# Kernel optimization log

Measured on AMD Instinct MI355X. Metric: run time of the kernel, lower is better.

## Reference

```python
import jax, jax.numpy as jnp
import numpy as np

N = 32768; G = 64; PER = N // G; E = 262144; H = 128; HEADS = 4; DH = H // HEADS

def _leaky(x):
    return jnp.where(x > 0, x, 0.01 * x)

def _bn(x, w, b, eps=1e-5):
    mu = jnp.mean(x, 0)
    var = jnp.var(x, 0)  # biased, as torch BatchNorm1d uses for normalization
    return (x - mu) * jax.lax.rsqrt(var + eps) * w + b

def setup_inputs():
    key = jax.random.key(0)
    ks = jax.random.split(key, 20)
    s = 0.05
    g = jax.random.randint(ks[0], (E,), 0, G)
    src = g * PER + jax.random.randint(ks[1], (E,), 0, PER)
    dst = g * PER + jax.random.randint(ks[2], (E,), 0, PER)
    return {
        'node_fts': jax.random.normal(ks[3], (N, H)),
        'edge_attr': jax.random.normal(ks[4], (E, H)),
        'graph_fts': jax.random.normal(ks[5], (G, H)),
        'hidden': jax.random.normal(ks[6], (N, H)),
        'W_ee': jax.random.normal(ks[7], (H, H)) * s, 'b_ee': jnp.zeros((H,)),
        'M0': jax.random.normal(ks[8], (6 * H, H)) * s,
        'M1': jax.random.normal(ks[9], (H, H)) * s,
        'M2': jax.random.normal(ks[10], (H, H)) * s,
        'M3': jax.random.normal(ks[11], (H, H)) * s,
        'U1': jax.random.normal(ks[12], (2 * H, H)) * s,
        'U2': jax.random.normal(ks[13], (H, H)) * s,
        'Wqkv': jax.random.normal(ks[14], (H, 3 * H)) * s, 'bqkv': jnp.zeros((3 * H,)),
        'Wo': jax.random.normal(ks[15], (H, H)) * s, 'bo': jnp.zeros((H,)),
        'bn1_w': jnp.ones((H,)), 'bn1_b': jnp.zeros((H,)),
        'bn2_w': jnp.ones((H,)), 'bn2_b': jnp.zeros((H,)),
        'bn3_w': jnp.ones((H,)), 'bn3_b': jnp.zeros((H,)),
        'W1': jax.random.normal(ks[16], (H, 2 * H)) * s, 'b1': jnp.zeros((2 * H,)),
        'W2': jax.random.normal(ks[17], (2 * H, H)) * s, 'b2': jnp.zeros((H,)),
        'edge_index': jnp.stack([src, dst]),
        'batch': jnp.arange(N, dtype=jnp.int32) // PER,
    }

def _forward(node_fts, edge_attr, graph_fts, hidden, W_ee, b_ee, M0, M1, M2, M3,
             U1, U2, Wqkv, bqkv, Wo, bo, bn1_w, bn1_b, bn2_w, bn2_b,
             bn3_w, bn3_b, W1, b1, W2, b2, edge_index, batch):
    src, dst = edge_index[0], edge_index[1]
    ea = edge_attr @ W_ee + b_ee                            # GPS.edge_emb  [E,H]
    z = jnp.concatenate([node_fts, hidden], axis=-1)        # [N,2H]
    gfi = graph_fts[batch[dst]]                             # graph_fts_i   [E,H]
    # MPNN message: cat(x_i, x_j, edge_attr, graph_fts_i) -> 4-layer MLP, no bias
    m = jnp.concatenate([z[dst], z[src], ea, gfi], axis=-1) # [E,6H]
    m = m @ M0
    m = _leaky(m) @ M1
    m = _leaky(m) @ M2
    m = _leaky(m) @ M3                                      # [E,H]
    agg = jax.ops.segment_max(m, dst, num_segments=N)
    agg = jnp.where(jnp.isfinite(agg), agg, 0.0)            # PyG max-aggr: 0 for empty segments
    h_local = z @ U1 + agg @ U2                             # MPNN.update (use_gate=False)
    h1 = _bn(h_local + node_fts, bn1_w, bn1_b)              # GPSConv residual + norm1
    # global multihead attention over dense per-graph batches (all graphs exactly PER nodes)
    xd = node_fts.reshape(G, PER, H)
    q, k, v = jnp.split(xd @ Wqkv + bqkv, 3, axis=-1)
    q = q.reshape(G, PER, HEADS, DH).transpose(0, 2, 1, 3)
    k = k.reshape(G, PER, HEADS, DH).transpose(0, 2, 1, 3)
    v = v.reshape(G, PER, HEADS, DH).transpose(0, 2, 1, 3)
    att = jax.nn.softmax(jnp.einsum('ghqd,ghkd->ghqk', q, k) / float(np.sqrt(DH)), axis=-1)
    o = jnp.einsum('ghqk,ghkd->ghqd', att, v).transpose(0, 2, 1, 3).reshape(N, H)
    o = o @ Wo + bo
    h2 = _bn(o + node_fts, bn2_w, bn2_b)                    # residual + norm2
    out = h1 + h2
    out = out + (jax.nn.relu(out @ W1 + b1) @ W2 + b2)      # GPSConv MLP residual
    return _bn(out, bn3_w, bn3_b)                           # norm3

def reference(node_fts, edge_attr, graph_fts, hidden, W_ee, b_ee, M0, M1, M2, M3,
              U1, U2, Wqkv, bqkv, Wo, bo, bn1_w, bn1_b, bn2_w, bn2_b,
              bn3_w, bn3_b, W1, b1, W2, b2, edge_index, batch):
    return _forward(node_fts, edge_attr, graph_fts, hidden, W_ee, b_ee, M0, M1, M2, M3,
                    U1, U2, Wqkv, bqkv, Wo, bo, bn1_w, bn1_b, bn2_w, bn2_b,
                    bn3_w, bn3_b, W1, b1, W2, b2, edge_index, batch)
```

## Files before the change

kernel.cpp:

```cpp
#include <hip/hip_runtime.h>

typedef unsigned short u16;
typedef unsigned int u32;

#define NN 32768
#define EE 262144
#define HH 128
#define INV_N (1.0f / 32768.0f)
#define BN_EPS 1e-5f
#define ENC_NEGINF 0x007FFFFFu

typedef __attribute__((ext_vector_type(8))) __bf16 bf16x8;
typedef __attribute__((ext_vector_type(2))) __bf16 bf16x2;
typedef __attribute__((ext_vector_type(4))) float f32x4;

#define OFF_WEE 0
#define OFF_M0 16384
#define OFF_M1 114688
#define OFF_M2 131072
#define OFF_M3 147456
#define OFF_U 163840
#define OFF_QKV 212992
#define OFF_WO 262144
#define OFF_W1T 278528
#define OFF_W2T 311296
#define WT_ELEMS 344064

#define WS_AGG 0u
#define WS_OUTB 0u
#define WS_Y3 8388608u
#define WS_QKV 16777216u
#define WS_PD 16777216u
#define WS_PS 25165824u
#define WS_Y1 16777216u
#define WS_Y2 25165824u
#define WS_STATS 41943040u
#define WS_WT 41946112u
#define WS_WC 42634240u
#define WS_BV 42667008u
#define WS_G 42667520u

__device__ __forceinline__ float bf2f(u16 u) {
  union { u32 u; float f; } x; x.u = ((u32)u) << 16; return x.f;
}
__device__ __forceinline__ u16 f2bf(float f) {
  union { float f; u32 u; } x; x.f = f;
  return (u16)((x.u + 0x7FFFu + ((x.u >> 16) & 1u)) >> 16);
}
__device__ __forceinline__ u32 pk2bf(float a, float b) {
#if __has_builtin(__builtin_amdgcn_cvt_pk_bf16_f32)
  bf16x2 r = __builtin_amdgcn_cvt_pk_bf16_f32(a, b);
  return __builtin_bit_cast(u32, r);
#else
  return (u32)f2bf(a) | ((u32)f2bf(b) << 16);
#endif
}
__device__ __forceinline__ u32 encf(float f) {
  union { float f; u32 u; } x; x.f = f;
  return (x.u & 0x80000000u) ? ~x.u : (x.u | 0x80000000u);
}
__device__ __forceinline__ float decf(u32 u) {
  union { u32 u; float f; } x;
  x.u = (u & 0x80000000u) ? (u ^ 0x80000000u) : ~u;
  return x.f;
}
__device__ __forceinline__ bf16x8 ld_frag(const u16* p) {
  return __builtin_bit_cast(bf16x8, *(const uint4*)p);
}
__device__ __forceinline__ uint4 pack8(const float* p) {
  float4 x = *(const float4*)p;
  float4 y = *(const float4*)(p + 4);
  return make_uint4(pk2bf(x.x, x.y), pk2bf(x.z, x.w), pk2bf(y.x, y.y),
                    pk2bf(y.z, y.w));
}

template <int NCT>
__device__ __forceinline__ void mfma_step(const u16* As, int astride, int ka,
                                          const u16* Ws, int wstride, int kw,
                                          f32x4* acc, int lane, int wrow) {
  const int q = lane >> 4, cl = lane & 15;
  bf16x8 a = ld_frag(As + (wrow + cl) * astride + ka + q * 8);
#pragma unroll
  for (int ct = 0; ct < NCT; ++ct) {
    bf16x8 b = ld_frag(Ws + (ct * 16 + cl) * wstride + kw + q * 8);
    acc[ct] = __builtin_amdgcn_mfma_f32_16x16x32_bf16(a, b, acc[ct], 0, 0, 0);
  }
}

template <int NCT>
__device__ __forceinline__ void mfma_chunk128(const u16* A0, const u16* A1,
                                              const u16* Ws, int wstride,
                                              f32x4* acc, int lane, int wrow) {
  mfma_step<NCT>(A0, 72, 0, Ws, wstride, 0, acc, lane, wrow);
  mfma_step<NCT>(A0, 72, 32, Ws, wstride, 32, acc, lane, wrow);
  mfma_step<NCT>(A1, 72, 0, Ws, wstride, 64, acc, lane, wrow);
  mfma_step<NCT>(A1, 72, 32, Ws, wstride, 96, acc, lane, wrow);
}

__device__ __forceinline__ void stageA64f(u16* dst, const float* src, int rs, int tid) {
#pragma unroll
  for (int i = 0; i < 2; ++i) {
    int idx = tid + i * 256, r = idx >> 3, s = idx & 7;
    *(uint4*)(dst + r * 72 + s * 8) = pack8(src + (size_t)r * rs + s * 8);
  }
}
__device__ __forceinline__ void stageA64(u16* dst, const u16* src, int rs, int tid) {
#pragma unroll
  for (int i = 0; i < 2; ++i) {
    int idx = tid + i * 256, r = idx >> 3, s = idx & 7;
    *(uint4*)(dst + r * 72 + s * 8) = *(const uint4*)(src + (size_t)r * rs + s * 8);
  }
}
__device__ __forceinline__ void stageA128(u16* dst, const u16* src, int tid) {
#pragma unroll
  for (int i = 0; i < 4; ++i) {
    int idx = tid + i * 256, r = idx >> 4, s = idx & 15;
    *(uint4*)(dst + r * 136 + s * 8) = *(const uint4*)(src + (size_t)r * HH + s * 8);
  }
}
template <int NR, int KW, int DS>
__device__ __forceinline__ void stageW(u16* dst, const u16* wt, int K, int koff, int tid) {
  constexpr int SEGS = KW / 8;
  constexpr int ITER = NR * SEGS / 256;
#pragma unroll
  for (int i = 0; i < ITER; ++i) {
    int idx = tid + i * 256;
    int c = idx / SEGS, s = idx % SEGS;
    *(uint4*)(dst + c * DS + s * 8) = *(const uint4*)(wt + (size_t)c * K + koff + s * 8);
  }
}
__device__ __forceinline__ void stage_agg(u16* dst, const u32* src, int tid) {
#pragma unroll
  for (int i = 0; i < 2; ++i) {
    int idx = tid + i * 256, r = idx >> 3, s = idx & 7;
    const u32* p = src + (size_t)r * HH + s * 8;
    u32 o[4];
#pragma unroll
    for (int j = 0; j < 4; ++j) {
      u32 u0 = p[2 * j], u1 = p[2 * j + 1];
      float f0 = (u0 == ENC_NEGINF) ? 0.f : decf(u0);
      float f1 = (u1 == ENC_NEGINF) ? 0.f : decf(u1);
      o[j] = pk2bf(f0, f1);
    }
    *(uint4*)(dst + r * 72 + s * 8) = make_uint4(o[0], o[1], o[2], o[3]);
  }
}


__global__ __launch_bounds__(256) void k_init(u32* __restrict__ agg,
                                              float* __restrict__ stats) {
  int gid = blockIdx.x * 256 + threadIdx.x;
  *(uint4*)(agg + (size_t)gid * 4) =
      make_uint4(ENC_NEGINF, ENC_NEGINF, ENC_NEGINF, ENC_NEGINF);
  if (gid < 768) stats[gid] = 0.f;
}

__global__ __launch_bounds__(256) void k_transpose(
    const float* w_ee, const float* m0, const float* m1, const float* m2,
    const float* m3, const float* u1, const float* u2, const float* wqkv,
    const float* wo, const float* w1, const float* w2, u16* __restrict__ wt) {
  const float* src; int K, C, ds, dk; size_t doff;
  switch (blockIdx.y) {
    case 0: src = w_ee; K = 128; C = 128; doff = OFF_WEE; ds = 128; dk = 0; break;
    case 1: src = m0; K = 768; C = 128; doff = OFF_M0; ds = 768; dk = 0; break;
    case 2: src = m1; K = 128; C = 128; doff = OFF_M1; ds = 128; dk = 0; break;
    case 3: src = m2; K = 128; C = 128; doff = OFF_M2; ds = 128; dk = 0; break;
    case 4: src = m3; K = 128; C = 128; doff = OFF_M3; ds = 128; dk = 0; break;
    case 5: src = u1; K = 256; C = 128; doff = OFF_U; ds = 384; dk = 0; break;
    case 6: src = u2; K = 128; C = 128; doff = OFF_U; ds = 384; dk = 256; break;
    case 7: src = wqkv; K = 128; C = 384; doff = OFF_QKV; ds = 128; dk = 0; break;
    case 8: src = wo; K = 128; C = 128; doff = OFF_WO; ds = 128; dk = 0; break;
    case 9: src = w1; K = 128; C = 256; doff = OFF_W1T; ds = 128; dk = 0; break;
    default: src = w2; K = 256; C = 128; doff = OFF_W2T; ds = 256; dk = 0; break;
  }
  int gid = blockIdx.x * 256 + threadIdx.x;
  if (gid < K * C) {
    int k = gid / C, c = gid - k * C;
    wt[doff + (size_t)c * ds + dk + k] = f2bf(src[gid]);
  }
}

__global__ __launch_bounds__(256) void k_prep(const float* __restrict__ b_ee,
                                              const float* __restrict__ graph_fts,
                                              const u16* __restrict__ wt,
                                              u16* __restrict__ wc,
                                              float* __restrict__ bv,
                                              float* __restrict__ G) {
  const int b = blockIdx.x, tid = threadIdx.x;
  if (b < 64) {
    int idx = b * 256 + tid, c = idx >> 7, k = idx & 127;
    const u16* m0 = wt + OFF_M0 + (size_t)c * 768 + 512;
    const u16* we = wt + OFF_WEE + k;
    float s = 0.f;
#pragma unroll 4
    for (int j = 0; j < 128; ++j) s += bf2f(we[j * 128]) * bf2f(m0[j]);
    wc[(size_t)c * 128 + k] = f2bf(s);
  } else if (b < 96) {
    int idx = (b - 64) * 256 + tid, g = idx >> 7, c = idx & 127;
    const u16* m0 = wt + OFF_M0 + (size_t)c * 768 + 640;
    const float* gf = graph_fts + (size_t)g * 128;
    float s = 0.f;
#pragma unroll 4
    for (int j = 0; j < 128; ++j) s += gf[j] * bf2f(m0[j]);
    G[(size_t)g * 128 + c] = s;
  } else if (tid < 128) {
    const u16* m0 = wt + OFF_M0 + (size_t)tid * 768 + 512;
    float s = 0.f;
#pragma unroll 4
    for (int j = 0; j < 128; ++j) s += b_ee[j] * bf2f(m0[j]);
    bv[tid] = s;
  }
}

__global__ __launch_bounds__(256) void k_pd(const float* __restrict__ nf,
                                            const float* __restrict__ hid,
                                            const float* __restrict__ bv,
                                            const float* __restrict__ G,
                                            const u16* __restrict__ wt,
                                            u16* __restrict__ pd,
                                            u16* __restrict__ ps) {
  __shared__ u16 sA0[64 * 72], sA1[64 * 72], sW[128 * 136];
  const int tid = threadIdx.x, lane = tid & 63, w = tid >> 6, wrow = w * 16;
  const int q = lane >> 4, cl = lane & 15;
  const int nb = blockIdx.x * 64, g = nb >> 9;
  const f32x4 fz = {0.f, 0.f, 0.f, 0.f};
  f32x4 accd[8], accs[8];
#pragma unroll
  for (int i = 0; i < 8; ++i) { accd[i] = fz; accs[i] = fz; }
  stageA64f(sA0, nf + (size_t)nb * HH, HH, tid);
  stageA64f(sA1, nf + (size_t)nb * HH + 64, HH, tid);
  stageW<128, 128, 136>(sW, wt + OFF_M0, 768, 0, tid);
  __syncthreads();
  mfma_chunk128<8>(sA0, sA1, sW, 136, accd, lane, wrow);
  __syncthreads();
  stageW<128, 128, 136>(sW, wt + OFF_M0, 768, 256, tid);
  __syncthreads();
  mfma_chunk128<8>(sA0, sA1, sW, 136, accs, lane, wrow);
  __syncthreads();
  stageA64f(sA0, hid + (size_t)nb * HH, HH, tid);
  stageA64f(sA1, hid + (size_t)nb * HH + 64, HH, tid);
  stageW<128, 128, 136>(sW, wt + OFF_M0, 768, 128, tid);
  __syncthreads();
  mfma_chunk128<8>(sA0, sA1, sW, 136, accd, lane, wrow);
  __syncthreads();
  stageW<128, 128, 136>(sW, wt + OFF_M0, 768, 384, tid);
  __syncthreads();
  mfma_chunk128<8>(sA0, sA1, sW, 136, accs, lane, wrow);
#pragma unroll
  for (int ct = 0; ct < 8; ++ct) {
#pragma unroll
    for (int r = 0; r < 4; ++r) {
      int row = wrow + q * 4 + r, col = ct * 16 + cl;
      size_t gi = (size_t)(nb + row) * HH + col;
      pd[gi] = f2bf(accd[ct][r] + G[(size_t)g * 128 + col] + bv[col]);
      ps[gi] = f2bf(accs[ct][r]);
    }
  }
}

#define ES 132
__device__ __forceinline__ void gemm4(f32x4* acc, const u16* sA, const u16* sB,
                                      int lane, int wrow) {
  mfma_step<8>(sA, ES, 0, sB, ES, 0, acc, lane, wrow);
  mfma_step<8>(sA, ES, 32, sB, ES, 32, acc, lane, wrow);
  mfma_step<8>(sA, ES, 64, sB, ES, 64, acc, lane, wrow);
  mfma_step<8>(sA, ES, 96, sB, ES, 96, acc, lane, wrow);
}
__device__ __forceinline__ void stageB(u16* sB, const u16* src, int tid) {
#pragma unroll
  for (int i = 0; i < 8; ++i) {
    int idx = tid + i * 256, c = idx >> 4, s = idx & 15;
    *(uint4*)(sB + c * ES + s * 8) = *(const uint4*)(src + (size_t)c * 128 + s * 8);
  }
}

__global__ __launch_bounds__(256, 3) void k_edge(
    const float* __restrict__ edge_attr, const u16* __restrict__ wc,
    const u16* __restrict__ pd, const u16* __restrict__ ps,
    const u16* __restrict__ wt, const int* __restrict__ ei,
    u32* __restrict__ agg) {
  __shared__ u16 sB[128 * ES];
  __shared__ u16 sA[64 * ES];
  __shared__ int sSrc[64], sDst[64];
  const int tid = threadIdx.x, lane = tid & 63, w = tid >> 6, wrow = w * 16;
  const int q = lane >> 4, cl = lane & 15;
  const int e0 = blockIdx.x * 64;
  if (tid < 64) {
    sSrc[tid] = ei[e0 + tid];
    sDst[tid] = ei[EE + e0 + tid];
  }
  {
    int r = tid >> 2, s = tid & 3;
    const float* p = edge_attr + (size_t)(e0 + r) * HH + s * 32;
#pragma unroll
    for (int k = 0; k < 4; ++k)
      *(uint4*)(sA + r * ES + s * 32 + k * 8) = pack8(p + k * 8);
  }
  stageB(sB, wc, tid);
  __syncthreads();
  const f32x4 fz = {0.f, 0.f, 0.f, 0.f};
  f32x4 acc[8];
#pragma unroll
  for (int i = 0; i < 8; ++i) acc[i] = fz;
  gemm4(acc, sA, sB, lane, wrow);
  __syncthreads();
  {
    int r = tid >> 2, s = tid & 3;
    const u16* prow = pd + (size_t)sDst[r] * HH + s * 32;
    const u16* srow = ps + (size_t)sSrc[r] * HH + s * 32;
#pragma unroll
    for (int k = 0; k < 4; ++k) {
      uint4 a = *(const uint4*)(prow + k * 8);
      uint4 b = *(const uint4*)(srow + k * 8);
      u32 ra[4] = {a.x, a.y, a.z, a.w}, rb[4] = {b.x, b.y, b.z, b.w};
      u32 o[4];
#pragma unroll
      for (int j = 0; j < 4; ++j) {
        float lo = bf2f((u16)ra[j]) + bf2f((u16)rb[j]);
        float hi = bf2f((u16)(ra[j] >> 16)) + bf2f((u16)(rb[j] >> 16));
        o[j] = pk2bf(lo, hi);
      }
      *(uint4*)(sA + r * ES + s * 32 + k * 8) = make_uint4(o[0], o[1], o[2], o[3]);
    }
  }
  stageB(sB, wt + OFF_M1, tid);
  __syncthreads();
#pragma unroll
  for (int ct = 0; ct < 8; ++ct)
#pragma unroll
    for (int r = 0; r < 4; ++r) {
      int off = (wrow + q * 4 + r) * ES + ct * 16 + cl;
      float v = acc[ct][r] + bf2f(sA[off]);
      v = v > 0.f ? v : 0.01f * v;
      sA[off] = f2bf(v);
    }
#pragma unroll
  for (int i = 0; i < 8; ++i) acc[i] = fz;
  gemm4(acc, sA, sB, lane, wrow);
  __syncthreads();
  stageB(sB, wt + OFF_M2, tid);
  __syncthreads();
#pragma unroll
  for (int ct = 0; ct < 8; ++ct)
#pragma unroll
    for (int r = 0; r < 4; ++r) {
      float v = acc[ct][r];
      v = v > 0.f ? v : 0.01f * v;
      sA[(wrow + q * 4 + r) * ES + ct * 16 + cl] = f2bf(v);
    }
#pragma unroll
  for (int i = 0; i < 8; ++i) acc[i] = fz;
  gemm4(acc, sA, sB, lane, wrow);
  __syncthreads();
  stageB(sB, wt + OFF_M3, tid);
  __syncthreads();
#pragma unroll
  for (int ct = 0; ct < 8; ++ct)
#pragma unroll
    for (int r = 0; r < 4; ++r) {
      float v = acc[ct][r];
      v = v > 0.f ? v : 0.01f * v;
      sA[(wrow + q * 4 + r) * ES + ct * 16 + cl] = f2bf(v);
    }
#pragma unroll
  for (int i = 0; i < 8; ++i) acc[i] = fz;
  gemm4(acc, sA, sB, lane, wrow);
#pragma unroll
  for (int r = 0; r < 4; ++r) {
    int d_r = sDst[wrow + q * 4 + r];
#pragma unroll
    for (int ct = 0; ct < 8; ++ct)
      atomicMax(&agg[(size_t)d_r * HH + ct * 16 + cl], encf(acc[ct][r]));
  }
}

__global__ __launch_bounds__(256) void k_y1(const float* __restrict__ node_fts,
                                            const float* __restrict__ hidden,
                                            const u32* __restrict__ agg,
                                            const u16* __restrict__ wt,
                                            u16* __restrict__ y1) {
  __shared__ u16 sA0[64 * 72], sA1[64 * 72], sW[128 * 136];
  const int tid = threadIdx.x, lane = tid & 63, w = tid >> 6, wrow = w * 16;
  const int q = lane >> 4, cl = lane & 15;
  const int nb = blockIdx.x * 64;
  const f32x4 fz = {0.f, 0.f, 0.f, 0.f};
  f32x4 acc[8];
#pragma unroll
  for (int i = 0; i < 8; ++i) acc[i] = fz;
  stageA64f(sA0, node_fts + (size_t)nb * HH, HH, tid);
  stageA64f(sA1, node_fts + (size_t)nb * HH + 64, HH, tid);
  stageW<128, 128, 136>(sW, wt + OFF_U, 384, 0, tid);
  __syncthreads();
  mfma_chunk128<8>(sA0, sA1, sW, 136, acc, lane, wrow);
  __syncthreads();
  stageA64f(sA0, hidden + (size_t)nb * HH, HH, tid);
  stageA64f(sA1, hidden + (size_t)nb * HH + 64, HH, tid);
  stageW<128, 128, 136>(sW, wt + OFF_U, 384, 128, tid);
  __syncthreads();
  mfma_chunk128<8>(sA0, sA1, sW, 136, acc, lane, wrow);
  __syncthreads();
  stage_agg(sA0, agg + (size_t)nb * HH, tid);
  stage_agg(sA1, agg + (size_t)nb * HH + 64, tid);
  stageW<128, 128, 136>(sW, wt + OFF_U, 384, 256, tid);
  __syncthreads();
  mfma_chunk128<8>(sA0, sA1, sW, 136, acc, lane, wrow);
#pragma unroll
  for (int ct = 0; ct < 8; ++ct) {
#pragma unroll
    for (int r = 0; r < 4; ++r) {
      int row = wrow + q * 4 + r, col = ct * 16 + cl;
      size_t gi = (size_t)(nb + row) * HH + col;
      y1[gi] = f2bf(acc[ct][r] + node_fts[gi]);
    }
  }
}

__global__ __launch_bounds__(256) void k_qkv(const float* __restrict__ node_fts,
                                             const u16* __restrict__ wt,
                                             const float* __restrict__ bqkv,
                                             u16* __restrict__ qkv) {
  __shared__ u16 sA0[64 * 72], sA1[64 * 72], sW[128 * 136];
  const int tid = threadIdx.x, lane = tid & 63, w = tid >> 6, wrow = w * 16;
  const int q = lane >> 4, cl = lane & 15;
  const int nb = blockIdx.x * 64;
  const f32x4 fz = {0.f, 0.f, 0.f, 0.f};
  stageA64f(sA0, node_fts + (size_t)nb * HH, HH, tid);
  stageA64f(sA1, node_fts + (size_t)nb * HH + 64, HH, tid);
#pragma unroll 1
  for (int cc = 0; cc < 3; ++cc) {
    if (cc) __syncthreads();
    stageW<128, 128, 136>(sW, wt + OFF_QKV + cc * 128 * 128, 128, 0, tid);
    __syncthreads();
    f32x4 acc[8];
#pragma unroll
    for (int i = 0; i < 8; ++i) acc[i] = fz;
    mfma_chunk128<8>(sA0, sA1, sW, 136, acc, lane, wrow);
#pragma unroll
    for (int ct = 0; ct < 8; ++ct) {
#pragma unroll
      for (int r = 0; r < 4; ++r) {
        int row = wrow + q * 4 + r, col = ct * 16 + cl;
        qkv[(size_t)(nb + row) * 384 + cc * 128 + col] =
            f2bf(acc[ct][r] + bqkv[cc * 128 + col]);
      }
    }
  }
}

#define SPW (32 * 136)
__global__ __launch_bounds__(256) void k_attn(const u16* __restrict__ qkv,
                                              u16* __restrict__ oatt) {
  __shared__ u16 sK[128 * 40];
  __shared__ u16 sVt[32 * 136];
  __shared__ u16 sP[4 * SPW];
  const int tid = threadIdx.x, lane = tid & 63, w = tid >> 6;
  const int q = lane >> 4, cl = lane & 15;
  const int bx = blockIdx.x;
  const int g = bx >> 4, h = (bx >> 2) & 3, qt = bx & 3;
  const u16* base = qkv + (size_t)g * 512 * 384;
  const int q0 = qt * 128 + w * 32;
  const float scale = 0.17677669529663687f;
  bf16x8 qa[2];
#pragma unroll
  for (int t = 0; t < 2; ++t)
    qa[t] = ld_frag(base + (size_t)(q0 + t * 16 + cl) * 384 + h * 32 + q * 8);
  const f32x4 fz = {0.f, 0.f, 0.f, 0.f};
  f32x4 accO[2][2];
  float m_[2][4], l_[2][4];
#pragma unroll
  for (int t = 0; t < 2; ++t) {
    accO[t][0] = fz;
    accO[t][1] = fz;
#pragma unroll
    for (int r = 0; r < 4; ++r) {
      m_[t][r] = -3.4e38f;
      l_[t][r] = 0.f;
    }
  }
  u16* myP = sP + w * SPW;
#pragma unroll 1
  for (int kt = 0; kt < 4; ++kt) {
    __syncthreads();
#pragma unroll
    for (int i = 0; i < 2; ++i) {
      int ii = tid + i * 256, r = ii >> 2, s = ii & 3;
      *(uint4*)(sK + r * 40 + s * 8) =
          *(const uint4*)(base + (size_t)(kt * 128 + r) * 384 + 128 + h * 32 + s * 8);
    }
#pragma unroll
    for (int i = 0; i < 2; ++i) {
      int ii = tid + i * 256, r = ii >> 2, s = ii & 3;
      uint4 v = *(const uint4*)(base + (size_t)(kt * 128 + r) * 384 + 256 + h * 32 + s * 8);
      u32 a[4] = {v.x, v.y, v.z, v.w};
#pragma unroll
      for (int j = 0; j < 4; ++j) {
        sVt[(s * 8 + 2 * j) * 136 + r] = (u16)a[j];
        sVt[(s * 8 + 2 * j + 1) * 136 + r] = (u16)(a[j] >> 16);
      }
    }
    __syncthreads();
    f32x4 accS[2][8];
#pragma unroll
    for (int ct = 0; ct < 8; ++ct) {
      bf16x8 b = ld_frag(sK + (ct * 16 + cl) * 40 + q * 8);
      accS[0][ct] = __builtin_amdgcn_mfma_f32_16x16x32_bf16(qa[0], b, fz, 0, 0, 0);
      accS[1][ct] = __builtin_amdgcn_mfma_f32_16x16x32_bf16(qa[1], b, fz, 0, 0, 0);
    }
#pragma unroll
    for (int t = 0; t < 2; ++t) {
#pragma unroll
      for (int r = 0; r < 4; ++r) {
        float mx = accS[t][0][r];
#pragma unroll
        for (int ct = 1; ct < 8; ++ct) mx = fmaxf(mx, accS[t][ct][r]);
        mx = fmaxf(mx, __shfl_xor(mx, 1));
        mx = fmaxf(mx, __shfl_xor(mx, 2));
        mx = fmaxf(mx, __shfl_xor(mx, 4));
        mx = fmaxf(mx, __shfl_xor(mx, 8));
        float mn = fmaxf(m_[t][r], mx * scale);
        float f = __expf(m_[t][r] - mn);
        m_[t][r] = mn;
        float rs = 0.f;
#pragma unroll
        for (int ct = 0; ct < 8; ++ct) {
          float p = __expf(accS[t][ct][r] * scale - mn);
          accS[t][ct][r] = p;
          rs += p;
        }
        rs += __shfl_xor(rs, 1);
        rs += __shfl_xor(rs, 2);
        rs += __shfl_xor(rs, 4);
        rs += __shfl_xor(rs, 8);
        l_[t][r] = l_[t][r] * f + rs;
        accO[t][0][r] *= f;
        accO[t][1][r] *= f;
      }
    }
#pragma unroll
    for (int t = 0; t < 2; ++t)
#pragma unroll
      for (int ct = 0; ct < 8; ++ct)
#pragma unroll
        for (int r = 0; r < 4; ++r)
          myP[(t * 16 + q * 4 + r) * 136 + ct * 16 + cl] = f2bf(accS[t][ct][r]);
#pragma unroll
    for (int kk = 0; kk < 4; ++kk) {
      bf16x8 pa0 = ld_frag(myP + (size_t)cl * 136 + kk * 32 + q * 8);
      bf16x8 pa1 = ld_frag(myP + (size_t)(16 + cl) * 136 + kk * 32 + q * 8);
#pragma unroll
      for (int c = 0; c < 2; ++c) {
        bf16x8 b = ld_frag(sVt + (c * 16 + cl) * 136 + kk * 32 + q * 8);
        accO[0][c] = __builtin_amdgcn_mfma_f32_16x16x32_bf16(pa0, b, accO[0][c], 0, 0, 0);
        accO[1][c] = __builtin_amdgcn_mfma_f32_16x16x32_bf16(pa1, b, accO[1][c], 0, 0, 0);
      }
    }
  }
#pragma unroll
  for (int t = 0; t < 2; ++t)
#pragma unroll
    for (int r = 0; r < 4; ++r) {
      float il = 1.f / l_[t][r];
      int row = g * 512 + q0 + t * 16 + q * 4 + r;
#pragma unroll
      for (int c = 0; c < 2; ++c)
        oatt[(size_t)row * HH + h * 32 + c * 16 + cl] = f2bf(accO[t][c][r] * il);
    }
}

__global__ __launch_bounds__(256) void k_y2(const u16* __restrict__ oatt,
                                            const float* __restrict__ node_fts,
                                            const u16* __restrict__ wt,
                                            const float* __restrict__ bo,
                                            u16* __restrict__ y2) {
  __shared__ u16 sA0[64 * 72], sA1[64 * 72], sW[128 * 136];
  const int tid = threadIdx.x, lane = tid & 63, w = tid >> 6, wrow = w * 16;
  const int q = lane >> 4, cl = lane & 15;
  const int nb = blockIdx.x * 64;
  const f32x4 fz = {0.f, 0.f, 0.f, 0.f};
  f32x4 acc[8];
#pragma unroll
  for (int i = 0; i < 8; ++i) acc[i] = fz;
  stageA64(sA0, oatt + (size_t)nb * HH, HH, tid);
  stageA64(sA1, oatt + (size_t)nb * HH + 64, HH, tid);
  stageW<128, 128, 136>(sW, wt + OFF_WO, 128, 0, tid);
  __syncthreads();
  mfma_chunk128<8>(sA0, sA1, sW, 136, acc, lane, wrow);
#pragma unroll
  for (int ct = 0; ct < 8; ++ct) {
#pragma unroll
    for (int r = 0; r < 4; ++r) {
      int row = wrow + q * 4 + r, col = ct * 16 + cl;
      size_t gi = (size_t)(nb + row) * HH + col;
      y2[gi] = f2bf(acc[ct][r] + bo[col] + node_fts[gi]);
    }
  }
}

__global__ __launch_bounds__(256) void k_stats(const u16* __restrict__ y,
                                               float* __restrict__ sum,
                                               float* __restrict__ sq) {
  const int tid = threadIdx.x, f = tid & 127, rh = tid >> 7;
  const int rb = blockIdx.x * 64;
  float s = 0.f, s2 = 0.f;
  for (int i = 0; i < 32; ++i) {
    float v = bf2f(y[(size_t)(rb + rh + 2 * i) * HH + f]);
    s += v;
    s2 += v * v;
  }
  __shared__ float bs[256], bq[256];
  bs[tid] = s;
  bq[tid] = s2;
  __syncthreads();
  if (tid < 128) {
    atomicAdd(&sum[f], bs[tid] + bs[tid + 128]);
    atomicAdd(&sq[f], bq[tid] + bq[tid + 128]);
  }
}

__global__ __launch_bounds__(256) void k_combine(
    const u16* __restrict__ y1, const u16* __restrict__ y2,
    const float* __restrict__ stats, const float* __restrict__ w1,
    const float* __restrict__ b1, const float* __restrict__ w2,
    const float* __restrict__ b2, u16* __restrict__ outb) {
  int i4 = blockIdx.x * 256 + threadIdx.x;
  uint2 a2 = *(const uint2*)(y1 + (size_t)i4 * 4);
  uint2 b2v = *(const uint2*)(y2 + (size_t)i4 * 4);
  u16 av[4] = {(u16)a2.x, (u16)(a2.x >> 16), (u16)a2.y, (u16)(a2.y >> 16)};
  u16 bv[4] = {(u16)b2v.x, (u16)(b2v.x >> 16), (u16)b2v.y, (u16)(b2v.y >> 16)};
  int f0 = (i4 & 31) * 4;
  u16 o[4];
#pragma unroll
  for (int j = 0; j < 4; ++j) {
    int f = f0 + j;
    float mu1 = stats[f] * INV_N;
    float v1 = stats[128 + f] * INV_N - mu1 * mu1;
    float r1 = rsqrtf(v1 + BN_EPS);
    float mu2 = stats[256 + f] * INV_N;
    float v2 = stats[384 + f] * INV_N - mu2 * mu2;
    float r2 = rsqrtf(v2 + BN_EPS);
    float val = (bf2f(av[j]) - mu1) * r1 * w1[f] + b1[f] +
                (bf2f(bv[j]) - mu2) * r2 * w2[f] + b2[f];
    o[j] = f2bf(val);
  }
  u32 lo2 = (u32)o[0] | ((u32)o[1] << 16);
  u32 hi2 = (u32)o[2] | ((u32)o[3] << 16);
  *(uint2*)(outb + (size_t)i4 * 4) = make_uint2(lo2, hi2);
}

__global__ __launch_bounds__(256) void k_mlp(const u16* __restrict__ outb,
                                             const u16* __restrict__ wt,
                                             const float* __restrict__ b1,
                                             const float* __restrict__ b2,
                                             u16* __restrict__ y3) {
  __shared__ u16 sA[64 * 136];
  __shared__ u16 sW[128 * 136];
  __shared__ u16 sI[64 * 72];
  const int tid = threadIdx.x, lane = tid & 63, w = tid >> 6, wrow = w * 16;
  const int q = lane >> 4, cl = lane & 15;
  const int nb = blockIdx.x * 64;
  const f32x4 fz = {0.f, 0.f, 0.f, 0.f};
  stageA128(sA, outb + (size_t)nb * HH, tid);
  f32x4 acc3[8];
#pragma unroll
  for (int i = 0; i < 8; ++i) acc3[i] = fz;
#pragma unroll 1
  for (int cc = 0; cc < 4; ++cc) {
    __syncthreads();
    stageW<64, 128, 136>(sW, wt + OFF_W1T + cc * 64 * 128, 128, 0, tid);
    __syncthreads();
    f32x4 a1[4];
#pragma unroll
    for (int i = 0; i < 4; ++i) a1[i] = fz;
    mfma_step<4>(sA, 136, 0, sW, 136, 0, a1, lane, wrow);
    mfma_step<4>(sA, 136, 32, sW, 136, 32, a1, lane, wrow);
    mfma_step<4>(sA, 136, 64, sW, 136, 64, a1, lane, wrow);
    mfma_step<4>(sA, 136, 96, sW, 136, 96, a1, lane, wrow);
#pragma unroll
    for (int ct = 0; ct < 4; ++ct) {
      float bias = b1[cc * 64 + ct * 16 + cl];
#pragma unroll
      for (int r = 0; r < 4; ++r) {
        float v = fmaxf(a1[ct][r] + bias, 0.f);
        sI[(wrow + q * 4 + r) * 72 + ct * 16 + cl] = f2bf(v);
      }
    }
    __syncthreads();
    stageW<128, 64, 72>(sW, wt + OFF_W2T, 256, cc * 64, tid);
    __syncthreads();
    mfma_step<8>(sI, 72, 0, sW, 72, 0, acc3, lane, wrow);
    mfma_step<8>(sI, 72, 32, sW, 72, 32, acc3, lane, wrow);
  }
#pragma unroll
  for (int ct = 0; ct < 8; ++ct) {
#pragma unroll
    for (int r = 0; r < 4; ++r) {
      int row = wrow + q * 4 + r, col = ct * 16 + cl;
      size_t gi = (size_t)(nb + row) * HH + col;
      y3[gi] = f2bf(acc3[ct][r] + b2[col] + bf2f(outb[gi]));
    }
  }
}

__global__ __launch_bounds__(256) void k_final(const u16* __restrict__ y3,
                                               const float* __restrict__ sum3,
                                               const float* __restrict__ sq3,
                                               const float* __restrict__ w3,
                                               const float* __restrict__ b3,
                                               float* __restrict__ out) {
  int i4 = blockIdx.x * 256 + threadIdx.x;
  uint2 a2 = *(const uint2*)(y3 + (size_t)i4 * 4);
  u16 av[4] = {(u16)a2.x, (u16)(a2.x >> 16), (u16)a2.y, (u16)(a2.y >> 16)};
  int f0 = (i4 & 31) * 4;
  float o[4];
#pragma unroll
  for (int j = 0; j < 4; ++j) {
    int f = f0 + j;
    float mu = sum3[f] * INV_N;
    float var = sq3[f] * INV_N - mu * mu;
    float r = rsqrtf(var + BN_EPS);
    o[j] = (bf2f(av[j]) - mu) * r * w3[f] + b3[f];
  }
  *(float4*)(out + (size_t)i4 * 4) = make_float4(o[0], o[1], o[2], o[3]);
}

extern "C" void kernel_launch(void* const* d_in, const int* in_sizes, int n_in,
                              void* d_out, int out_size, void* d_ws, size_t ws_size,
                              hipStream_t stream) {
  (void)in_sizes; (void)n_in; (void)out_size; (void)ws_size;
  const float* node_fts = (const float*)d_in[0];
  const float* edge_attr = (const float*)d_in[1];
  const float* graph_fts = (const float*)d_in[2];
  const float* hidden = (const float*)d_in[3];
  const float* W_ee = (const float*)d_in[4];
  const float* b_ee = (const float*)d_in[5];
  const float* M0 = (const float*)d_in[6];
  const float* M1 = (const float*)d_in[7];
  const float* M2 = (const float*)d_in[8];
  const float* M3 = (const float*)d_in[9];
  const float* U1 = (const float*)d_in[10];
  const float* U2 = (const float*)d_in[11];
  const float* Wqkv = (const float*)d_in[12];
  const float* bqkv = (const float*)d_in[13];
  const float* Wo = (const float*)d_in[14];
  const float* bo = (const float*)d_in[15];
  const float* bn1w = (const float*)d_in[16];
  const float* bn1b = (const float*)d_in[17];
  const float* bn2w = (const float*)d_in[18];
  const float* bn2b = (const float*)d_in[19];
  const float* bn3w = (const float*)d_in[20];
  const float* bn3b = (const float*)d_in[21];
  const float* W1 = (const float*)d_in[22];
  const float* b1 = (const float*)d_in[23];
  const float* W2 = (const float*)d_in[24];
  const float* b2 = (const float*)d_in[25];
  const int* ei = (const int*)d_in[26];

  char* ws = (char*)d_ws;
  u32* agg = (u32*)(ws + WS_AGG);
  u16* outb = (u16*)(ws + WS_OUTB);
  u16* y3 = (u16*)(ws + WS_Y3);
  u16* qkv = (u16*)(ws + WS_QKV);
  u16* pd = (u16*)(ws + WS_PD);
  u16* ps = (u16*)(ws + WS_PS);
  u16* y1 = (u16*)(ws + WS_Y1);
  u16* y2 = (u16*)(ws + WS_Y2);
  float* stats = (float*)(ws + WS_STATS);
  u16* wt = (u16*)(ws + WS_WT);
  u16* wc = (u16*)(ws + WS_WC);
  float* bv = (float*)(ws + WS_BV);
  float* G = (float*)(ws + WS_G);
  u16* oatt = (u16*)d_out;
  float* out = (float*)d_out;

  k_init<<<4096, 256, 0, stream>>>(agg, stats);
  k_transpose<<<dim3(384, 11), 256, 0, stream>>>(W_ee, M0, M1, M2, M3, U1, U2,
                                                 Wqkv, Wo, W1, W2, wt);
  k_prep<<<97, 256, 0, stream>>>(b_ee, graph_fts, wt, wc, bv, G);
  k_pd<<<512, 256, 0, stream>>>(node_fts, hidden, bv, G, wt, pd, ps);
  k_edge<<<4096, 256, 0, stream>>>(edge_attr, wc, pd, ps, wt, ei, agg);
  k_qkv<<<512, 256, 0, stream>>>(node_fts, wt, bqkv, qkv);
  k_attn<<<1024, 256, 0, stream>>>(qkv, oatt);
  k_y1<<<512, 256, 0, stream>>>(node_fts, hidden, agg, wt, y1);
  k_y2<<<512, 256, 0, stream>>>(oatt, node_fts, wt, bo, y2);
  k_stats<<<512, 256, 0, stream>>>(y1, stats + 0, stats + 128);
  k_stats<<<512, 256, 0, stream>>>(y2, stats + 256, stats + 384);
  k_combine<<<4096, 256, 0, stream>>>(y1, y2, stats, bn1w, bn1b, bn2w, bn2b, outb);
  k_mlp<<<512, 256, 0, stream>>>(outb, wt, b1, b2, y3);
  k_stats<<<512, 256, 0, stream>>>(y3, stats + 512, stats + 640);
  k_final<<<4096, 256, 0, stream>>>(y3, stats + 512, stats + 640, bn3w, bn3b, out);
}
```

Measured before the change: 711.3 us.

## Counting-sort edges by destination and pre-reduce segment max before atomics

Adds histogram, scan and scatter kernels that counting-sort edges by destination node on every call. The edge kernel then gathers edge_attr, src and dst in sorted order. Each wave first reduces runs of equal destination in shared memory, so it issues atomicMax only once per destination segment instead of once per edge element. This is meant to cut the very large number of global atomics. The costs are three extra launches including a single-block scan, a random-row gather of edge_attr, and rounding the final values to bf16 before the max.

New measurement: 763.2 us. 7.3% more time.

```diff
diff --git a/kernel.cpp b/kernel.cpp
--- a/kernel.cpp
+++ b/kernel.cpp
@@ -39,6 +39,11 @@
 #define WS_WC 42634240u
 #define WS_BV 42667008u
 #define WS_G 42667520u
+#define WS_HIST 42700800u
+#define WS_CUR 42831872u
+#define WS_SE 42962944u
+#define WS_SSRC 44011520u
+#define WS_SDST 45060096u
 
 __device__ __forceinline__ float bf2f(u16 u) {
   union { u32 u; float f; } x; x.u = ((u32)u) << 16; return x.f;
@@ -148,11 +153,55 @@
 
 
 __global__ __launch_bounds__(256) void k_init(u32* __restrict__ agg,
-                                              float* __restrict__ stats) {
+                                              float* __restrict__ stats,
+                                              u32* __restrict__ hist) {
   int gid = blockIdx.x * 256 + threadIdx.x;
   *(uint4*)(agg + (size_t)gid * 4) =
       make_uint4(ENC_NEGINF, ENC_NEGINF, ENC_NEGINF, ENC_NEGINF);
   if (gid < 768) stats[gid] = 0.f;
+  if (gid < 32768) hist[gid] = 0;
+}
+
+__global__ __launch_bounds__(256) void k_hist(const int* __restrict__ ei,
+                                              u32* __restrict__ hist) {
+  int e = blockIdx.x * 256 + threadIdx.x;
+  atomicAdd(&hist[ei[EE + e]], 1u);
+}
+
+__global__ __launch_bounds__(1024) void k_scan(const u32* __restrict__ hist,
+                                               u32* __restrict__ cursor) {
+  __shared__ u32 part[1024];
+  const int t = threadIdx.x;
+  u32 pre[32], sum = 0;
+#pragma unroll
+  for (int i = 0; i < 32; ++i) {
+    pre[i] = sum;
+    sum += hist[t * 32 + i];
+  }
+  part[t] = sum;
+  __syncthreads();
+  for (int off = 1; off < 1024; off <<= 1) {
+    u32 v = (t >= off) ? part[t - off] : 0;
+    __syncthreads();
+    part[t] += v;
+    __syncthreads();
+  }
+  u32 base = part[t] - sum;
+#pragma unroll
+  for (int i = 0; i < 32; ++i) cursor[t * 32 + i] = base + pre[i];
+}
+
+__global__ __launch_bounds__(256) void k_scatter(const int* __restrict__ ei,
+                                                 u32* __restrict__ cursor,
+                                                 int* __restrict__ sE,
+                                                 int* __restrict__ sSrc,
+                                                 int* __restrict__ sDst) {
+  int e = blockIdx.x * 256 + threadIdx.x;
+  int d = ei[EE + e];
+  u32 pos = atomicAdd(&cursor[d], 1u);
+  sE[pos] = e;
+  sSrc[pos] = ei[e];
+  sDst[pos] = d;
 }
 
 __global__ __launch_bounds__(256) void k_transpose(
@@ -277,21 +326,19 @@
 __global__ __launch_bounds__(256, 3) void k_edge(
     const float* __restrict__ edge_attr, const u16* __restrict__ wc,
     const u16* __restrict__ pd, const u16* __restrict__ ps,
-    const u16* __restrict__ wt, const int* __restrict__ ei,
+    const u16* __restrict__ wt, const int* __restrict__ sE,
+    const int* __restrict__ sSrcG, const int* __restrict__ sDstG,
     u32* __restrict__ agg) {
   __shared__ u16 sB[128 * ES];
   __shared__ u16 sA[64 * ES];
-  __shared__ int sSrc[64], sDst[64];
+  __shared__ int sDst[64];
   const int tid = threadIdx.x, lane = tid & 63, w = tid >> 6, wrow = w * 16;
   const int q = lane >> 4, cl = lane & 15;
   const int e0 = blockIdx.x * 64;
-  if (tid < 64) {
-    sSrc[tid] = ei[e0 + tid];
-    sDst[tid] = ei[EE + e0 + tid];
-  }
+  if (tid < 64) sDst[tid] = sDstG[e0 + tid];
   {
     int r = tid >> 2, s = tid & 3;
-    const float* p = edge_attr + (size_t)(e0 + r) * HH + s * 32;
+    const float* p = edge_attr + (size_t)sE[e0 + r] * HH + s * 32;
 #pragma unroll
     for (int k = 0; k < 4; ++k)
       *(uint4*)(sA + r * ES + s * 32 + k * 8) = pack8(p + k * 8);
@@ -306,8 +353,8 @@
   __syncthreads();
   {
     int r = tid >> 2, s = tid & 3;
-    const u16* prow = pd + (size_t)sDst[r] * HH + s * 32;
-    const u16* srow = ps + (size_t)sSrc[r] * HH + s * 32;
+    const u16* prow = pd + (size_t)sDstG[e0 + r] * HH + s * 32;
+    const u16* srow = ps + (size_t)sSrcG[e0 + r] * HH + s * 32;
 #pragma unroll
     for (int k = 0; k < 4; ++k) {
       uint4 a = *(const uint4*)(prow + k * 8);
@@ -366,11 +413,28 @@
   for (int i = 0; i < 8; ++i) acc[i] = fz;
   gemm4(acc, sA, sB, lane, wrow);
 #pragma unroll
-  for (int r = 0; r < 4; ++r) {
-    int d_r = sDst[wrow + q * 4 + r];
-#pragma unroll
-    for (int ct = 0; ct < 8; ++ct)
-      atomicMax(&agg[(size_t)d_r * HH + ct * 16 + cl], encf(acc[ct][r]));
+  for (int ct = 0; ct < 8; ++ct)
+#pragma unroll
+    for (int r = 0; r < 4; ++r)
+      sA[(wrow + q * 4 + r) * ES + ct * 16 + cl] = f2bf(acc[ct][r]);
+  {
+    float run0 = -3.4e38f, run1 = -3.4e38f;
+    int prev = sDst[wrow];
+#pragma unroll
+    for (int i = 0; i < 16; ++i) {
+      int d = sDst[wrow + i];
+      if (d != prev) {
+        atomicMax(&agg[(size_t)prev * HH + lane], encf(run0));
+        atomicMax(&agg[(size_t)prev * HH + 64 + lane], encf(run1));
+        run0 = -3.4e38f;
+        run1 = -3.4e38f;
+        prev = d;
+      }
+      run0 = fmaxf(run0, bf2f(sA[(wrow + i) * ES + lane]));
+      run1 = fmaxf(run1, bf2f(sA[(wrow + i) * ES + 64 + lane]));
+    }
+    atomicMax(&agg[(size_t)prev * HH + lane], encf(run0));
+    atomicMax(&agg[(size_t)prev * HH + 64 + lane], encf(run1));
   }
 }
 
@@ -769,15 +833,23 @@
   u16* wc = (u16*)(ws + WS_WC);
   float* bv = (float*)(ws + WS_BV);
   float* G = (float*)(ws + WS_G);
+  u32* hist = (u32*)(ws + WS_HIST);
+  u32* cursor = (u32*)(ws + WS_CUR);
+  int* sE = (int*)(ws + WS_SE);
+  int* sSrc = (int*)(ws + WS_SSRC);
+  int* sDst = (int*)(ws + WS_SDST);
   u16* oatt = (u16*)d_out;
   float* out = (float*)d_out;
 
-  k_init<<<4096, 256, 0, stream>>>(agg, stats);
+  k_init<<<4096, 256, 0, stream>>>(agg, stats, hist);
+  k_hist<<<1024, 256, 0, stream>>>(ei, hist);
+  k_scan<<<1, 1024, 0, stream>>>(hist, cursor);
+  k_scatter<<<1024, 256, 0, stream>>>(ei, cursor, sE, sSrc, sDst);
   k_transpose<<<dim3(384, 11), 256, 0, stream>>>(W_ee, M0, M1, M2, M3, U1, U2,
                                                  Wqkv, Wo, W1, W2, wt);
   k_prep<<<97, 256, 0, stream>>>(b_ee, graph_fts, wt, wc, bv, G);
   k_pd<<<512, 256, 0, stream>>>(node_fts, hidden, bv, G, wt, pd, ps);
-  k_edge<<<4096, 256, 0, stream>>>(edge_attr, wc, pd, ps, wt, ei, agg);
+  k_edge<<<4096, 256, 0, stream>>>(edge_attr, wc, pd, ps, wt, sE, sSrc, sDst, agg);
   k_qkv<<<512, 256, 0, stream>>>(node_fts, wt, bqkv, qkv);
   k_attn<<<1024, 256, 0, stream>>>(qkv, oatt);
   k_y1<<<512, 256, 0, stream>>>(node_fts, hidden, agg, wt, y1);
```
